# Kernel tuning notes

Hardware: AMD Instinct MI355X
Metric: run time of the kernel (lower is better)

Reference implementation:

```python
import jax, jax.numpy as jnp
import numpy as np

N = 100000          # nodes
E = 1600000         # edges (avg degree 16)
F_IN = 128          # input node features
H1, C1 = 8, 8       # conv1: 8 heads, 8 channels/head -> 64 concat
NUM_CLASSES = 40    # conv2: 1 head, 40 channels
EPS = 1e-16         # PyG softmax denominator epsilon
NEG_SLOPE = 0.2     # PyG GATConv default leaky_relu slope


def setup_inputs() -> dict:
    key = jax.random.key(0)
    ks = jax.random.split(key, 12)
    x = jax.random.normal(ks[0], (N, F_IN), jnp.float32)
    edge_index = jax.random.randint(ks[1], (2, E), 0, N, dtype=jnp.int64)
    edge_attr = jax.random.normal(ks[2], (E, 1), jnp.float32)
    # layer 1 params (Glorot-ish scaling)
    s1 = 1.0 / np.sqrt(F_IN)
    W1 = jax.random.normal(ks[3], (F_IN, H1 * C1), jnp.float32) * s1
    a_src1 = jax.random.normal(ks[4], (H1, C1), jnp.float32) * (1.0 / np.sqrt(C1))
    a_dst1 = jax.random.normal(ks[5], (H1, C1), jnp.float32) * (1.0 / np.sqrt(C1))
    b1 = jnp.zeros((H1 * C1,), jnp.float32)
    # layer 2 params: in = 64 (conv1 concat output), 1 head, NUM_CLASSES channels
    s2 = 1.0 / np.sqrt(H1 * C1)
    W2 = jax.random.normal(ks[6], (H1 * C1, NUM_CLASSES), jnp.float32) * s2
    a_src2 = jax.random.normal(ks[7], (1, NUM_CLASSES), jnp.float32) * (1.0 / np.sqrt(NUM_CLASSES))
    a_dst2 = jax.random.normal(ks[8], (1, NUM_CLASSES), jnp.float32) * (1.0 / np.sqrt(NUM_CLASSES))
    b2 = jnp.zeros((NUM_CLASSES,), jnp.float32)
    return {"x": x, "edge_index": edge_index, "edge_attr": edge_attr,
            "W1": W1, "a_src1": a_src1, "a_dst1": a_dst1, "b1": b1,
            "W2": W2, "a_src2": a_src2, "a_dst2": a_dst2, "b2": b2}


def gat_conv(x, src, dst, W, a_s, a_d, b, heads, out_ch):
    """PyG GATConv: linear -> per-edge leaky-relu attention -> dst softmax -> scatter-add."""
    n = x.shape[0]
    h = (x @ W).reshape(n, heads, out_ch)                 # [N,H,C]
    alpha_s = jnp.sum(h * a_s, axis=-1)                   # [N,H]
    alpha_d = jnp.sum(h * a_d, axis=-1)                   # [N,H]
    e = jax.nn.leaky_relu(alpha_s[src] + alpha_d[dst], NEG_SLOPE)  # [Etot,H]
    # segment softmax over incoming edges per destination node
    m = jax.ops.segment_max(e, dst, num_segments=n)       # [N,H]
    e = jnp.exp(e - m[dst])
    denom = jax.ops.segment_sum(e, dst, num_segments=n)   # [N,H]
    alpha = e / (denom[dst] + EPS)                        # [Etot,H]
    msg = h[src] * alpha[:, :, None]                      # [Etot,H,C]
    out = jax.ops.segment_sum(msg, dst, num_segments=n)   # [N,H,C]
    return out.reshape(n, heads * out_ch) + b             # concat heads + bias


def reference(x, edge_index, edge_attr, W1, a_src1, a_dst1, b1, W2, a_src2, a_dst2, b2):
    n = x.shape[0]
    # PyG GATConv adds self-loops by default
    loops = jnp.arange(n, dtype=edge_index.dtype)
    src = jnp.concatenate([edge_index[0], loops])
    dst = jnp.concatenate([edge_index[1], loops])
    x = x.astype(jnp.float32)
    x1 = jax.nn.elu(gat_conv(x, src, dst, W1, a_src1, a_dst1, b1, H1, C1))
    x2 = jax.nn.elu(gat_conv(x1, src, dst, W2, a_src2, a_dst2, b2, 1, NUM_CLASSES))
    return x2
```

## Files before the change

### kernel.cpp

```cpp
#include <hip/hip_runtime.h>
#include <math.h>

#define NN 100000
#define NE 1600000
#define NETOT (NE + NN)
#define FIN 128
#define H1N 8
#define D1 64
#define NC 40
#define LNT 64
#define LOG2E 1.44269504088896f

#define BSH 9
#define BNODES 512
#define NBUC ((NN + BNODES - 1) / BNODES)
#define EPB 4096
#define NBLKA ((NE + EPB - 1) / EPB)
#define BCAP 9216
#define LB1 ((NN + LNT - 1) / LNT)

__device__ __forceinline__ float leakyf(float x) { return x >= 0.0f ? x : 0.2f * x; }
__device__ __forceinline__ float eluf(float x)   { return x > 0.0f ? x : expm1f(x); }
__device__ __forceinline__ float exp2fast(float x) { return __builtin_amdgcn_exp2f(x); }

__device__ __forceinline__ unsigned short f2bf(float f) {
  unsigned u = __float_as_uint(f);
  u += 0x7fffu + ((u >> 16) & 1u);
  return (unsigned short)(u >> 16);
}
__device__ __forceinline__ float bflo(unsigned u) { return __uint_as_float(u << 16); }
__device__ __forceinline__ float bfhi(unsigned u) { return __uint_as_float(u & 0xffff0000u); }

__global__ void k_detect(const long long* __restrict__ ei, int* __restrict__ flag) {
  if (blockIdx.x == 0 && threadIdx.x == 0) {
    int is64 = 1;
    for (int i = 0; i < 16; ++i) {
      long long v = ei[i];
      if (v < 0 || v >= NN) is64 = 0;
    }
    *flag = is64;
  }
}

#define XS1(node, k) xs[(node) * FIN + ((k) ^ ((node) & 31))]
__global__ __launch_bounds__(512) void k_fusedA(
    const void* __restrict__ ei, const int* __restrict__ flag,
    unsigned int* __restrict__ subbuf, int* __restrict__ bcnt,
    const float* __restrict__ x, const float* __restrict__ W,
    const float* __restrict__ aw_s, const float* __restrict__ aw_d,
    unsigned short* __restrict__ h, float* __restrict__ als,
    float* __restrict__ ald) {
  __shared__ __align__(16) char smem[65536];
  int t = threadIdx.x;
  if (blockIdx.x < NBLKA) {
    unsigned int*   pay    = (unsigned int*)smem;
    unsigned int*   spay   = pay + EPB;
    unsigned short* bk     = (unsigned short*)(spay + EPB);
    unsigned short* sbk    = bk + EPB;
    int*            hist   = (int*)(sbk + EPB);
    int*            lstart = hist + 256;
    int*            cur    = lstart + 256;
    int*            gbase  = cur + 256;
    int e0 = blockIdx.x * EPB;
    int cnt = min(EPB, NE - e0);
    if (t < 256) hist[t] = 0;
    __syncthreads();
    bool f64 = (*flag) != 0;
    for (int i = t; i < cnt; i += 512) {
      int s, d;
      if (f64) {
        const long long* p = (const long long*)ei;
        s = (int)p[e0 + i]; d = (int)p[NE + e0 + i];
      } else {
        const int* p = (const int*)ei;
        s = p[e0 + i]; d = p[NE + e0 + i];
      }
      int b = d >> BSH;
      pay[i] = ((unsigned)s << BSH) | (unsigned)(d & (BNODES - 1));
      bk[i] = (unsigned short)b;
      atomicAdd(&hist[b], 1);
    }
    __syncthreads();
    int v = 0;
    if (t < 256) { v = hist[t]; lstart[t] = v; }
    __syncthreads();
    for (int st = 1; st < 256; st <<= 1) {
      int xv = (t < 256 && t >= st) ? lstart[t - st] : 0;
      __syncthreads();
      if (t < 256) lstart[t] += xv;
      __syncthreads();
    }
    int excl = 0;
    if (t < 256) excl = lstart[t] - v;
    __syncthreads();
    if (t < 256) {
      lstart[t] = excl;
      cur[t] = excl;
      gbase[t] = (v > 0) ? atomicAdd(&bcnt[t], v) : 0;
    }
    __syncthreads();
    for (int i = t; i < cnt; i += 512) {
      int b = bk[i];
      int pos = atomicAdd(&cur[b], 1);
      spay[pos] = pay[i];
      sbk[pos] = (unsigned short)b;
    }
    __syncthreads();
    for (int i = t; i < cnt; i += 512) {
      int b = sbk[i];
      int o = gbase[b] + (i - lstart[b]);
      if (o < BCAP) subbuf[(size_t)b * BCAP + o] = spay[i];
    }
  } else {
    float* ws = (float*)smem;
    float* xs = ws + FIN * D1;
    int base = (blockIdx.x - NBLKA) * LNT;
    for (int i = t; i < FIN * D1; i += 512) ws[i] = W[i];
    for (int i = t; i < LNT * FIN; i += 512) {
      int node = i >> 7, k = i & 127;
      int gn = base + node;
      if (gn >= NN) gn = NN - 1;
      XS1(node, k) = x[(size_t)gn * FIN + k];
    }
    __syncthreads();
    int head = t & 7, nl = t >> 3;
    float acc[8] = {0, 0, 0, 0, 0, 0, 0, 0};
    #pragma unroll 4
    for (int k = 0; k < FIN; ++k) {
      float x0 = XS1(nl, k);
      const float4* wr = (const float4*)&ws[k * D1 + head * 8];
      float4 wa = wr[0], wb = wr[1];
      acc[0] = fmaf(x0, wa.x, acc[0]);
      acc[1] = fmaf(x0, wa.y, acc[1]);
      acc[2] = fmaf(x0, wa.z, acc[2]);
      acc[3] = fmaf(x0, wa.w, acc[3]);
      acc[4] = fmaf(x0, wb.x, acc[4]);
      acc[5] = fmaf(x0, wb.y, acc[5]);
      acc[6] = fmaf(x0, wb.z, acc[6]);
      acc[7] = fmaf(x0, wb.w, acc[7]);
    }
    int n0 = base + nl;
    if (n0 < NN) {
      float s = 0.f, d = 0.f;
      #pragma unroll
      for (int c = 0; c < 8; ++c) {
        h[(size_t)n0 * D1 + head * 8 + c] = f2bf(acc[c]);
        s = fmaf(acc[c], aw_s[head * 8 + c], s);
        d = fmaf(acc[c], aw_d[head * 8 + c], d);
      }
      als[n0 * H1N + head] = s * LOG2E;
      ald[n0 * H1N + head] = d * LOG2E;
    }
  }
}

__global__ void k_bucketsum(const int* __restrict__ bcnt, int* __restrict__ bucket_base,
                            int* __restrict__ row_start) {
  __shared__ int sh[256];
  int t = threadIdx.x;
  int tot = 0;
  if (t < NBUC) {
    int d0 = t << BSH;
    int nloc = min(BNODES, NN - d0);
    tot = nloc + min(bcnt[t], BCAP);
  }
  sh[t] = tot;
  __syncthreads();
  for (int s = 1; s < 256; s <<= 1) {
    int x = (t >= s) ? sh[t - s] : 0;
    __syncthreads();
    sh[t] += x;
    __syncthreads();
  }
  if (t < NBUC) bucket_base[t] = sh[t] - tot;
  if (t == NBUC - 1) row_start[NN] = sh[t];
}

__global__ __launch_bounds__(256) void k_passB(const int* __restrict__ bcnt,
                       const unsigned int* __restrict__ subbuf,
                       const int* __restrict__ bucket_base,
                       int* __restrict__ row_start, int* __restrict__ csr) {
  __shared__ int hist[BNODES];
  __shared__ int ps[256];
  __shared__ int cur[BNODES];
  int b = blockIdx.x, t = threadIdx.x;
  int d0 = b << BSH;
  int nloc = min(BNODES, NN - d0);
  hist[t] = 0; hist[t + 256] = 0;
  __syncthreads();
  int cnt = min(bcnt[b], BCAP);
  const unsigned int* sb = subbuf + (size_t)b * BCAP;
  for (int i = t; i < cnt; i += 256)
    atomicAdd(&hist[sb[i] & (BNODES - 1)], 1);
  __syncthreads();
  int j0 = 2 * t, j1 = 2 * t + 1;
  int s0 = (j0 < nloc) ? hist[j0] + 1 : 0;
  int s1 = (j1 < nloc) ? hist[j1] + 1 : 0;
  int pairsum = s0 + s1;
  ps[t] = pairsum;
  __syncthreads();
  for (int s = 1; s < 256; s <<= 1) {
    int x = (t >= s) ? ps[t - s] : 0;
    __syncthreads();
    ps[t] += x;
    __syncthreads();
  }
  int excl = ps[t] - pairsum + bucket_base[b];
  if (j0 < nloc) {
    row_start[d0 + j0] = excl;
    csr[excl] = d0 + j0;
    cur[j0] = excl + 1;
  }
  if (j1 < nloc) {
    int rs = excl + s0;
    row_start[d0 + j1] = rs;
    csr[rs] = d0 + j1;
    cur[j1] = rs + 1;
  }
  __syncthreads();
  for (int i = t; i < cnt; i += 256) {
    unsigned u = sb[i];
    int pos = atomicAdd(&cur[u & (BNODES - 1)], 1);
    csr[pos] = (int)(u >> BSH);
  }
}

#define XS2(node, k) xs[(node) * D1 + ((k) ^ ((node) & 31))]
__global__ __launch_bounds__(512) void k_lin2(
    const unsigned int* __restrict__ x1bf, const float* __restrict__ W,
    const float* __restrict__ aw_s, const float* __restrict__ aw_d,
    unsigned short* __restrict__ h, float* __restrict__ als,
    float* __restrict__ ald) {
  __shared__ float ws[D1 * D1];
  __shared__ float xs[LNT * D1];
  int t = threadIdx.x;
  int base = blockIdx.x * LNT;
  for (int i = t; i < D1 * D1; i += 512) {
    int k = i >> 6, c = i & 63;
    ws[i] = (c < NC) ? W[k * NC + c] : 0.f;
  }
  for (int i = t; i < LNT * 32; i += 512) {
    int node = i >> 5, kd = i & 31;
    int gn = base + node;
    if (gn >= NN) gn = NN - 1;
    unsigned u = x1bf[(size_t)gn * 32 + kd];
    XS2(node, 2 * kd)     = bflo(u);
    XS2(node, 2 * kd + 1) = bfhi(u);
  }
  __syncthreads();
  int g = t & 7, nl = t >> 3;
  float acc[8] = {0, 0, 0, 0, 0, 0, 0, 0};
  #pragma unroll 4
  for (int k = 0; k < D1; ++k) {
    float x0 = XS2(nl, k);
    const float4* wr = (const float4*)&ws[k * D1 + g * 8];
    float4 wa = wr[0], wb = wr[1];
    acc[0] = fmaf(x0, wa.x, acc[0]);
    acc[1] = fmaf(x0, wa.y, acc[1]);
    acc[2] = fmaf(x0, wa.z, acc[2]);
    acc[3] = fmaf(x0, wa.w, acc[3]);
    acc[4] = fmaf(x0, wb.x, acc[4]);
    acc[5] = fmaf(x0, wb.y, acc[5]);
    acc[6] = fmaf(x0, wb.z, acc[6]);
    acc[7] = fmaf(x0, wb.w, acc[7]);
  }
  int n0 = base + nl;
  float s = 0.f, d = 0.f;
  #pragma unroll
  for (int c = 0; c < 8; ++c) {
    int col = g * 8 + c;
    float aws = (col < NC) ? aw_s[col] : 0.f;
    float awd = (col < NC) ? aw_d[col] : 0.f;
    s = fmaf(acc[c], aws, s);
    d = fmaf(acc[c], awd, d);
  }
  s += __shfl_xor(s, 1); d += __shfl_xor(d, 1);
  s += __shfl_xor(s, 2); d += __shfl_xor(d, 2);
  s += __shfl_xor(s, 4); d += __shfl_xor(d, 4);
  if (n0 < NN) {
    if (g < 5) {
      #pragma unroll
      for (int c = 0; c < 8; ++c) h[(size_t)n0 * NC + g * 8 + c] = f2bf(acc[c]);
    }
    if (g == 0) { als[n0] = s * LOG2E; ald[n0] = d * LOG2E; }
  }
}

__global__ void k_node1(const int* __restrict__ row_start, const int* __restrict__ csr,
                        const unsigned short* __restrict__ h, const float* __restrict__ als,
                        const float* __restrict__ ald, const float* __restrict__ b,
                        unsigned int* __restrict__ x1bf) {
  __shared__ float pl[4][2][32 * 9];
  int wid = threadIdx.x >> 6, half = (threadIdx.x >> 5) & 1, c2 = threadIdx.x & 31;
  int n = blockIdx.x * 8 + wid * 2 + half;
  float* pw = pl[wid][half];
  const unsigned int* h32 = (const unsigned int*)h;
  int r0 = row_start[n], r1 = row_start[n + 1];
  int hd = c2 >> 2;
  const float4* adp = (const float4*)(ald + (size_t)n * H1N);
  float4 ad0 = adp[0], ad1 = adp[1];
  float S = 0.f;
  float alo0 = 0.f, ahi0 = 0.f, alo1 = 0.f, ahi1 = 0.f;
  float alo2 = 0.f, ahi2 = 0.f, alo3 = 0.f, ahi3 = 0.f;
  for (int kb = r0; kb < r1; kb += 32) {
    int cnt = min(32, r1 - kb);
    if (c2 < cnt) {
      int sk = csr[kb + c2];
      const float4* ap = (const float4*)(als + (size_t)sk * H1N);
      float4 a0 = ap[0], a1 = ap[1];
      pw[c2 * 9 + 0] = exp2fast(leakyf(a0.x + ad0.x));
      pw[c2 * 9 + 1] = exp2fast(leakyf(a0.y + ad0.y));
      pw[c2 * 9 + 2] = exp2fast(leakyf(a0.z + ad0.z));
      pw[c2 * 9 + 3] = exp2fast(leakyf(a0.w + ad0.w));
      pw[c2 * 9 + 4] = exp2fast(leakyf(a1.x + ad1.x));
      pw[c2 * 9 + 5] = exp2fast(leakyf(a1.y + ad1.y));
      pw[c2 * 9 + 6] = exp2fast(leakyf(a1.z + ad1.z));
      pw[c2 * 9 + 7] = exp2fast(leakyf(a1.w + ad1.w));
      pw[c2 * 9 + 8] = __int_as_float(sk);
    }
    asm volatile("s_waitcnt lgkmcnt(0)" ::: "memory");
    int j = 0;
    for (; j + 4 <= cnt; j += 4) {
      int s0 = __float_as_int(pw[(j + 0) * 9 + 8]);
      int s1 = __float_as_int(pw[(j + 1) * 9 + 8]);
      int s2 = __float_as_int(pw[(j + 2) * 9 + 8]);
      int s3 = __float_as_int(pw[(j + 3) * 9 + 8]);
      float p0 = pw[(j + 0) * 9 + hd], p1 = pw[(j + 1) * 9 + hd];
      float p2 = pw[(j + 2) * 9 + hd], p3 = pw[(j + 3) * 9 + hd];
      unsigned u0 = h32[(unsigned)s0 * 32 + c2];
      unsigned u1 = h32[(unsigned)s1 * 32 + c2];
      unsigned u2 = h32[(unsigned)s2 * 32 + c2];
      unsigned u3 = h32[(unsigned)s3 * 32 + c2];
      alo0 = fmaf(p0, bflo(u0), alo0); ahi0 = fmaf(p0, bfhi(u0), ahi0);
      alo1 = fmaf(p1, bflo(u1), alo1); ahi1 = fmaf(p1, bfhi(u1), ahi1);
      alo2 = fmaf(p2, bflo(u2), alo2); ahi2 = fmaf(p2, bfhi(u2), ahi2);
      alo3 = fmaf(p3, bflo(u3), alo3); ahi3 = fmaf(p3, bfhi(u3), ahi3);
      S += (p0 + p1) + (p2 + p3);
    }
    for (; j < cnt; ++j) {
      int s0 = __float_as_int(pw[j * 9 + 8]);
      float p0 = pw[j * 9 + hd];
      unsigned u0 = h32[(unsigned)s0 * 32 + c2];
      alo0 = fmaf(p0, bflo(u0), alo0); ahi0 = fmaf(p0, bfhi(u0), ahi0);
      S += p0;
    }
  }
  float alo = (alo0 + alo1) + (alo2 + alo3);
  float ahi = (ahi0 + ahi1) + (ahi2 + ahi3);
  float inv = 1.0f / (S + 1e-16f);
  float ox = eluf(alo * inv + b[2 * c2 + 0]);
  float oy = eluf(ahi * inv + b[2 * c2 + 1]);
  x1bf[(size_t)n * 32 + c2] = (unsigned)f2bf(ox) | ((unsigned)f2bf(oy) << 16);
}

__global__ void k_node2(const int* __restrict__ row_start, const int* __restrict__ csr,
                        const unsigned short* __restrict__ h, const float* __restrict__ als,
                        const float* __restrict__ ald, const float* __restrict__ b,
                        float* __restrict__ out) {
  __shared__ float pl[4][2][32 * 3];
  int wid = threadIdx.x >> 6, half = (threadIdx.x >> 5) & 1, c2 = threadIdx.x & 31;
  int n = blockIdx.x * 8 + wid * 2 + half;
  float* pw = pl[wid][half];
  const unsigned int* h32 = (const unsigned int*)h;
  int r0 = row_start[n], r1 = row_start[n + 1];
  int cl = c2 < 20 ? c2 : 19;
  float aldn = ald[n];
  float S = 0.f;
  float alo0 = 0.f, ahi0 = 0.f, alo1 = 0.f, ahi1 = 0.f;
  float alo2 = 0.f, ahi2 = 0.f, alo3 = 0.f, ahi3 = 0.f;
  for (int kb = r0; kb < r1; kb += 32) {
    int cnt = min(32, r1 - kb);
    if (c2 < cnt) {
      int sk = csr[kb + c2];
      pw[c2 * 3 + 0] = exp2fast(leakyf(als[sk] + aldn));
      pw[c2 * 3 + 1] = __int_as_float(sk);
    }
    asm volatile("s_waitcnt lgkmcnt(0)" ::: "memory");
    int j = 0;
    for (; j + 4 <= cnt; j += 4) {
      int s0 = __float_as_int(pw[(j + 0) * 3 + 1]);
      int s1 = __float_as_int(pw[(j + 1) * 3 + 1]);
      int s2 = __float_as_int(pw[(j + 2) * 3 + 1]);
      int s3 = __float_as_int(pw[(j + 3) * 3 + 1]);
      float p0 = pw[(j + 0) * 3], p1 = pw[(j + 1) * 3];
      float p2 = pw[(j + 2) * 3], p3 = pw[(j + 3) * 3];
      unsigned u0 = h32[(unsigned)s0 * 20 + cl];
      unsigned u1 = h32[(unsigned)s1 * 20 + cl];
      unsigned u2 = h32[(unsigned)s2 * 20 + cl];
      unsigned u3 = h32[(unsigned)s3 * 20 + cl];
      alo0 = fmaf(p0, bflo(u0), alo0); ahi0 = fmaf(p0, bfhi(u0), ahi0);
      alo1 = fmaf(p1, bflo(u1), alo1); ahi1 = fmaf(p1, bfhi(u1), ahi1);
      alo2 = fmaf(p2, bflo(u2), alo2); ahi2 = fmaf(p2, bfhi(u2), ahi2);
      alo3 = fmaf(p3, bflo(u3), alo3); ahi3 = fmaf(p3, bfhi(u3), ahi3);
      S += (p0 + p1) + (p2 + p3);
    }
    for (; j < cnt; ++j) {
      int s0 = __float_as_int(pw[j * 3 + 1]);
      float p0 = pw[j * 3];
      unsigned u0 = h32[(unsigned)s0 * 20 + cl];
      alo0 = fmaf(p0, bflo(u0), alo0); ahi0 = fmaf(p0, bfhi(u0), ahi0);
      S += p0;
    }
  }
  float alo = (alo0 + alo1) + (alo2 + alo3);
  float ahi = (ahi0 + ahi1) + (ahi2 + ahi3);
  if (c2 < 20) {
    float inv = 1.0f / (S + 1e-16f);
    float2 o;
    o.x = eluf(alo * inv + b[2 * c2 + 0]);
    o.y = eluf(ahi * inv + b[2 * c2 + 1]);
    ((float2*)out)[(size_t)n * 20 + c2] = o;
  }
}

extern "C" void kernel_launch(void* const* d_in, const int* in_sizes, int n_in,
                              void* d_out, int out_size, void* d_ws, size_t ws_size,
                              hipStream_t stream) {
  const float* x    = (const float*)d_in[0];
  const void*  ei   = d_in[1];
  const float* W1   = (const float*)d_in[3];
  const float* as1w = (const float*)d_in[4];
  const float* ad1w = (const float*)d_in[5];
  const float* b1   = (const float*)d_in[6];
  const float* W2   = (const float*)d_in[7];
  const float* as2w = (const float*)d_in[8];
  const float* ad2w = (const float*)d_in[9];
  const float* b2   = (const float*)d_in[10];
  float* out = (float*)d_out;

  char* w = (char*)d_ws;
  size_t off = 0;
  auto carve = [&](size_t bytes) -> void* {
    void* r = w + off;
    off += (bytes + 255) & ~(size_t)255;
    return r;
  };
  int*            flag        = (int*)carve(256);
  int*            bcnt        = (int*)carve((size_t)NBUC * 4);
  int*            bucket_base = (int*)carve((size_t)NBUC * 4);
  unsigned int*   subbuf      = (unsigned int*)carve((size_t)NBUC * BCAP * 4);
  int*            row_start   = (int*)carve((size_t)(NN + 1) * 4);
  int*            csr         = (int*)carve((size_t)NETOT * 4);
  unsigned short* h1          = (unsigned short*)carve((size_t)NN * D1 * 2);
  float*          als1        = (float*)carve((size_t)NN * H1N * 4);
  float*          ald1        = (float*)carve((size_t)NN * H1N * 4);
  unsigned int*   x1bf        = (unsigned int*)carve((size_t)NN * 32 * 4);
  unsigned short* h2 = h1; float* als2 = als1; float* ald2 = ald1;

  k_detect<<<1, 64, 0, stream>>>((const long long*)ei, flag);
  (void)hipMemsetAsync(bcnt, 0, (size_t)NBUC * 4, stream);

  k_fusedA<<<NBLKA + LB1, 512, 0, stream>>>(ei, flag, subbuf, bcnt,
                                            x, W1, as1w, ad1w, h1, als1, ald1);

  k_bucketsum<<<1, 256, 0, stream>>>(bcnt, bucket_base, row_start);
  k_passB<<<NBUC, 256, 0, stream>>>(bcnt, subbuf, bucket_base, row_start, csr);

  k_node1<<<NN / 8, 256, 0, stream>>>(row_start, csr, h1, als1, ald1, b1, x1bf);

  k_lin2<<<LB1, 512, 0, stream>>>(x1bf, W2, as2w, ad2w, h2, als2, ald2);
  k_node2<<<NN / 8, 256, 0, stream>>>(row_start, csr, h2, als2, ald2, b2, out);
}
```

Measured before the change: 206.2 us.

## Fold memset and bucket scan into neighbours; register-tile layer-1 GEMM with bf16 x

Zeroing of the bucket counters moves into the detect kernel, replacing the memset. The separate bucket-prefix-sum kernel is removed and every passB block recomputes the scan redundantly, which cuts two launches from the stream. The layer-1 linear part of the fused kernel now handles 128 nodes per block, stores x in shared memory as swizzled bf16 pairs, and has each thread compute a 4-node by 4-channel register tile with a shuffle reduction for the attention logits. This adds an extra bf16 rounding of the input features and a redundant scan in each passB block.

```diff
diff --git a/kernel.cpp b/kernel.cpp
--- a/kernel.cpp
+++ b/kernel.cpp
@@ -9,6 +9,7 @@
 #define D1 64
 #define NC 40
 #define LNT 64
+#define LNT1 128
 #define LOG2E 1.44269504088896f
 
 #define BSH 9
@@ -17,7 +18,8 @@
 #define EPB 4096
 #define NBLKA ((NE + EPB - 1) / EPB)
 #define BCAP 9216
-#define LB1 ((NN + LNT - 1) / LNT)
+#define LB1A ((NN + LNT1 - 1) / LNT1)
+#define LB2  ((NN + LNT - 1) / LNT)
 
 __device__ __forceinline__ float leakyf(float x) { return x >= 0.0f ? x : 0.2f * x; }
 __device__ __forceinline__ float eluf(float x)   { return x > 0.0f ? x : expm1f(x); }
@@ -31,8 +33,11 @@
 __device__ __forceinline__ float bflo(unsigned u) { return __uint_as_float(u << 16); }
 __device__ __forceinline__ float bfhi(unsigned u) { return __uint_as_float(u & 0xffff0000u); }
 
-__global__ void k_detect(const long long* __restrict__ ei, int* __restrict__ flag) {
-  if (blockIdx.x == 0 && threadIdx.x == 0) {
+__global__ void k_detect(const long long* __restrict__ ei, int* __restrict__ flag,
+                         int* __restrict__ bcnt) {
+  int t = threadIdx.x;
+  if (t < NBUC) bcnt[t] = 0;
+  if (t == 0) {
     int is64 = 1;
     for (int i = 0; i < 16; ++i) {
       long long v = ei[i];
@@ -113,79 +118,115 @@
     }
   } else {
     float* ws = (float*)smem;
-    float* xs = ws + FIN * D1;
-    int base = (blockIdx.x - NBLKA) * LNT;
+    unsigned short* xs16 = (unsigned short*)(ws + FIN * D1);
+    unsigned int* xs32 = (unsigned int*)xs16;
+    int base = (blockIdx.x - NBLKA) * LNT1;
     for (int i = t; i < FIN * D1; i += 512) ws[i] = W[i];
-    for (int i = t; i < LNT * FIN; i += 512) {
-      int node = i >> 7, k = i & 127;
+    for (int i = t; i < LNT1 * (FIN / 4); i += 512) {
+      int node = i >> 5, q = i & 31;
       int gn = base + node;
       if (gn >= NN) gn = NN - 1;
-      XS1(node, k) = x[(size_t)gn * FIN + k];
-    }
-    __syncthreads();
-    int head = t & 7, nl = t >> 3;
-    float acc[8] = {0, 0, 0, 0, 0, 0, 0, 0};
+      float4 f = ((const float4*)(x + (size_t)gn * FIN))[q];
+      int np = node >> 1, hh = node & 1;
+      int k0 = 4 * q;
+      xs16[(k0 + 0) * LNT1 + (((np ^ ((k0 + 0) & 31)) << 1) | hh)] = f2bf(f.x);
+      xs16[(k0 + 1) * LNT1 + (((np ^ ((k0 + 1) & 31)) << 1) | hh)] = f2bf(f.y);
+      xs16[(k0 + 2) * LNT1 + (((np ^ ((k0 + 2) & 31)) << 1) | hh)] = f2bf(f.z);
+      xs16[(k0 + 3) * LNT1 + (((np ^ ((k0 + 3) & 31)) << 1) | hh)] = f2bf(f.w);
+    }
+    __syncthreads();
+    int cg = t & 15, np0 = t >> 4, np1 = np0 + 32;
+    float a0[4] = {0, 0, 0, 0}, a1[4] = {0, 0, 0, 0};
+    float a2[4] = {0, 0, 0, 0}, a3[4] = {0, 0, 0, 0};
     #pragma unroll 4
     for (int k = 0; k < FIN; ++k) {
-      float x0 = XS1(nl, k);
-      const float4* wr = (const float4*)&ws[k * D1 + head * 8];
-      float4 wa = wr[0], wb = wr[1];
-      acc[0] = fmaf(x0, wa.x, acc[0]);
-      acc[1] = fmaf(x0, wa.y, acc[1]);
-      acc[2] = fmaf(x0, wa.z, acc[2]);
-      acc[3] = fmaf(x0, wa.w, acc[3]);
-      acc[4] = fmaf(x0, wb.x, acc[4]);
-      acc[5] = fmaf(x0, wb.y, acc[5]);
-      acc[6] = fmaf(x0, wb.z, acc[6]);
-      acc[7] = fmaf(x0, wb.w, acc[7]);
-    }
-    int n0 = base + nl;
-    if (n0 < NN) {
-      float s = 0.f, d = 0.f;
-      #pragma unroll
-      for (int c = 0; c < 8; ++c) {
-        h[(size_t)n0 * D1 + head * 8 + c] = f2bf(acc[c]);
-        s = fmaf(acc[c], aw_s[head * 8 + c], s);
-        d = fmaf(acc[c], aw_d[head * 8 + c], d);
-      }
-      als[n0 * H1N + head] = s * LOG2E;
-      ald[n0 * H1N + head] = d * LOG2E;
-    }
-  }
-}
-
-__global__ void k_bucketsum(const int* __restrict__ bcnt, int* __restrict__ bucket_base,
-                            int* __restrict__ row_start) {
-  __shared__ int sh[256];
-  int t = threadIdx.x;
-  int tot = 0;
-  if (t < NBUC) {
-    int d0 = t << BSH;
-    int nloc = min(BNODES, NN - d0);
-    tot = nloc + min(bcnt[t], BCAP);
-  }
-  sh[t] = tot;
-  __syncthreads();
-  for (int s = 1; s < 256; s <<= 1) {
-    int x = (t >= s) ? sh[t - s] : 0;
-    __syncthreads();
-    sh[t] += x;
-    __syncthreads();
-  }
-  if (t < NBUC) bucket_base[t] = sh[t] - tot;
-  if (t == NBUC - 1) row_start[NN] = sh[t];
+      unsigned u0 = xs32[k * (LNT1 / 2) + (np0 ^ (k & 31))];
+      unsigned u1 = xs32[k * (LNT1 / 2) + (np1 ^ (k & 31))];
+      float xa = bflo(u0), xb = bfhi(u0);
+      float xc = bflo(u1), xd = bfhi(u1);
+      float4 wq = *(const float4*)&ws[k * D1 + cg * 4];
+      a0[0] = fmaf(xa, wq.x, a0[0]); a1[0] = fmaf(xb, wq.x, a1[0]);
+      a2[0] = fmaf(xc, wq.x, a2[0]); a3[0] = fmaf(xd, wq.x, a3[0]);
+      a0[1] = fmaf(xa, wq.y, a0[1]); a1[1] = fmaf(xb, wq.y, a1[1]);
+      a2[1] = fmaf(xc, wq.y, a2[1]); a3[1] = fmaf(xd, wq.y, a3[1]);
+      a0[2] = fmaf(xa, wq.z, a0[2]); a1[2] = fmaf(xb, wq.z, a1[2]);
+      a2[2] = fmaf(xc, wq.z, a2[2]); a3[2] = fmaf(xd, wq.z, a3[2]);
+      a0[3] = fmaf(xa, wq.w, a0[3]); a1[3] = fmaf(xb, wq.w, a1[3]);
+      a2[3] = fmaf(xc, wq.w, a2[3]); a3[3] = fmaf(xd, wq.w, a3[3]);
+    }
+    float aws[4], awd[4];
+    #pragma unroll
+    for (int c = 0; c < 4; ++c) { aws[c] = aw_s[cg * 4 + c]; awd[c] = aw_d[cg * 4 + c]; }
+    float s0 = 0, d0 = 0, s1 = 0, d1 = 0, s2 = 0, d2 = 0, s3 = 0, d3 = 0;
+    #pragma unroll
+    for (int c = 0; c < 4; ++c) {
+      s0 = fmaf(a0[c], aws[c], s0); d0 = fmaf(a0[c], awd[c], d0);
+      s1 = fmaf(a1[c], aws[c], s1); d1 = fmaf(a1[c], awd[c], d1);
+      s2 = fmaf(a2[c], aws[c], s2); d2 = fmaf(a2[c], awd[c], d2);
+      s3 = fmaf(a3[c], aws[c], s3); d3 = fmaf(a3[c], awd[c], d3);
+    }
+    s0 += __shfl_xor(s0, 1); d0 += __shfl_xor(d0, 1);
+    s1 += __shfl_xor(s1, 1); d1 += __shfl_xor(d1, 1);
+    s2 += __shfl_xor(s2, 1); d2 += __shfl_xor(d2, 1);
+    s3 += __shfl_xor(s3, 1); d3 += __shfl_xor(d3, 1);
+    int head = cg >> 1;
+    bool wlog = (cg & 1) == 0;
+    int nA = base + 2 * np0, nB = nA + 1;
+    int nC = base + 2 * np1, nD = nC + 1;
+    if (nA < NN) {
+      *(uint2*)(void*)(h + (size_t)nA * D1 + cg * 4) = make_uint2(
+        (unsigned)f2bf(a0[0]) | ((unsigned)f2bf(a0[1]) << 16),
+        (unsigned)f2bf(a0[2]) | ((unsigned)f2bf(a0[3]) << 16));
+      if (wlog) { als[nA * H1N + head] = s0 * LOG2E; ald[nA * H1N + head] = d0 * LOG2E; }
+    }
+    if (nB < NN) {
+      *(uint2*)(void*)(h + (size_t)nB * D1 + cg * 4) = make_uint2(
+        (unsigned)f2bf(a1[0]) | ((unsigned)f2bf(a1[1]) << 16),
+        (unsigned)f2bf(a1[2]) | ((unsigned)f2bf(a1[3]) << 16));
+      if (wlog) { als[nB * H1N + head] = s1 * LOG2E; ald[nB * H1N + head] = d1 * LOG2E; }
+    }
+    if (nC < NN) {
+      *(uint2*)(void*)(h + (size_t)nC * D1 + cg * 4) = make_uint2(
+        (unsigned)f2bf(a2[0]) | ((unsigned)f2bf(a2[1]) << 16),
+        (unsigned)f2bf(a2[2]) | ((unsigned)f2bf(a2[3]) << 16));
+      if (wlog) { als[nC * H1N + head] = s2 * LOG2E; ald[nC * H1N + head] = d2 * LOG2E; }
+    }
+    if (nD < NN) {
+      *(uint2*)(void*)(h + (size_t)nD * D1 + cg * 4) = make_uint2(
+        (unsigned)f2bf(a3[0]) | ((unsigned)f2bf(a3[1]) << 16),
+        (unsigned)f2bf(a3[2]) | ((unsigned)f2bf(a3[3]) << 16));
+      if (wlog) { als[nD * H1N + head] = s3 * LOG2E; ald[nD * H1N + head] = d3 * LOG2E; }
+    }
+  }
 }
 
 __global__ __launch_bounds__(256) void k_passB(const int* __restrict__ bcnt,
                        const unsigned int* __restrict__ subbuf,
-                       const int* __restrict__ bucket_base,
                        int* __restrict__ row_start, int* __restrict__ csr) {
   __shared__ int hist[BNODES];
   __shared__ int ps[256];
   __shared__ int cur[BNODES];
+  __shared__ int bbs;
   int b = blockIdx.x, t = threadIdx.x;
   int d0 = b << BSH;
   int nloc = min(BNODES, NN - d0);
+  int tot = 0;
+  if (t < NBUC) {
+    int dd = t << BSH;
+    tot = min(BNODES, NN - dd) + min(bcnt[t], BCAP);
+  }
+  ps[t] = tot;
+  __syncthreads();
+  for (int s = 1; s < 256; s <<= 1) {
+    int xv = (t >= s) ? ps[t - s] : 0;
+    __syncthreads();
+    ps[t] += xv;
+    __syncthreads();
+  }
+  if (t == 0) bbs = (b == 0) ? 0 : ps[b - 1];
+  if (b == 0 && t == 0) row_start[NN] = ps[NBUC - 1];
+  __syncthreads();
+  int bucket_base = bbs;
   hist[t] = 0; hist[t + 256] = 0;
   __syncthreads();
   int cnt = min(bcnt[b], BCAP);
@@ -205,7 +246,7 @@
     ps[t] += x;
     __syncthreads();
   }
-  int excl = ps[t] - pairsum + bucket_base[b];
+  int excl = ps[t] - pairsum + bucket_base;
   if (j0 < nloc) {
     row_start[d0 + j0] = excl;
     csr[excl] = d0 + j0;
@@ -437,7 +478,6 @@
   };
   int*            flag        = (int*)carve(256);
   int*            bcnt        = (int*)carve((size_t)NBUC * 4);
-  int*            bucket_base = (int*)carve((size_t)NBUC * 4);
   unsigned int*   subbuf      = (unsigned int*)carve((size_t)NBUC * BCAP * 4);
   int*            row_start   = (int*)carve((size_t)(NN + 1) * 4);
   int*            csr         = (int*)carve((size_t)NETOT * 4);
@@ -447,17 +487,15 @@
   unsigned int*   x1bf        = (unsigned int*)carve((size_t)NN * 32 * 4);
   unsigned short* h2 = h1; float* als2 = als1; float* ald2 = ald1;
 
-  k_detect<<<1, 64, 0, stream>>>((const long long*)ei, flag);
-  (void)hipMemsetAsync(bcnt, 0, (size_t)NBUC * 4, stream);
-
-  k_fusedA<<<NBLKA + LB1, 512, 0, stream>>>(ei, flag, subbuf, bcnt,
-                                            x, W1, as1w, ad1w, h1, als1, ald1);
-
-  k_bucketsum<<<1, 256, 0, stream>>>(bcnt, bucket_base, row_start);
-  k_passB<<<NBUC, 256, 0, stream>>>(bcnt, subbuf, bucket_base, row_start, csr);
+  k_detect<<<1, 256, 0, stream>>>((const long long*)ei, flag, bcnt);
+
+  k_fusedA<<<NBLKA + LB1A, 512, 0, stream>>>(ei, flag, subbuf, bcnt,
+                                             x, W1, as1w, ad1w, h1, als1, ald1);
+
+  k_passB<<<NBUC, 256, 0, stream>>>(bcnt, subbuf, row_start, csr);
 
   k_node1<<<NN / 8, 256, 0, stream>>>(row_start, csr, h1, als1, ald1, b1, x1bf);
 
-  k_lin2<<<LB1, 512, 0, stream>>>(x1bf, W2, as2w, ad2w, h2, als2, ald2);
+  k_lin2<<<LB2, 512, 0, stream>>>(x1bf, W2, as2w, ad2w, h2, als2, ald2);
   k_node2<<<NN / 8, 256, 0, stream>>>(row_start, csr, h2, als2, ald2, b2, out);
 }
```

Result: no change. 207.1 us (+0.4%).
